# Optimization experiments

Measured on AMD Instinct MI355X. Metric: run time of the kernel, lower is better.

## Reference

```python
import jax, jax.numpy as jnp
import numpy as np

B, N, T = 1024, 8192, 11  # batch, max atoms, atom types


def setup_inputs() -> dict:
    key = jax.random.key(0)
    k1, k2, k3 = jax.random.split(key, 3)
    input_coords = jax.random.normal(k1, (B, 3 * N), dtype=jnp.float32)
    atom_types = jax.random.randint(k2, (B, N), 0, T, dtype=jnp.int32)
    num_atoms = jax.random.randint(k3, (B,), 0, N, dtype=jnp.int32)
    return {"input_coords": input_coords, "atom_types": atom_types, "num_atoms": num_atoms}


def reference(input_coords, atom_types, num_atoms):
    # input_coords: [B, 3N], atom_types: [B, N] in [0, T), num_atoms: [B]
    b, n3 = input_coords.shape
    n = n3 // 3
    valid = jnp.arange(n)[None, :] < num_atoms[:, None]          # [B, N]
    # padded atoms get a sentinel type T so they sort to the end
    t_eff = jnp.where(valid, atom_types, T)                       # [B, N]
    # stable sort by type = contiguous per-type buckets, original order kept within type
    perm = jnp.argsort(t_eff, axis=1)                             # [B, N] (stable)
    coords3 = input_coords.reshape(b, n, 3)
    out = jnp.take_along_axis(coords3, perm[:, :, None], axis=1)  # [B, N, 3]
    valid_sorted = jnp.take_along_axis(valid, perm, axis=1)       # [B, N]
    out = out * valid_sorted[:, :, None].astype(out.dtype)        # zero padded slots
    # per-type counts and exclusive-prefix offsets
    counts_all = jnp.sum(jax.nn.one_hot(t_eff, T + 1, dtype=jnp.int32), axis=1)  # [B, T+1]
    num_atoms_of_type = counts_all[:, :T]                         # [B, T]
    offsets = jnp.concatenate(
        [jnp.zeros((b, 1), jnp.int32), jnp.cumsum(num_atoms_of_type, axis=1)[:, :-1]], axis=1
    )                                                              # [B, T]
    return out.reshape(b, n3), num_atoms_of_type, offsets
```

## Files before the change

kernel.cpp:

```cpp
#include <hip/hip_runtime.h>

#define NB 512
#define APT 16
#define NTYPE 11
#define CPAD 13
#define NATOMS 8192
#define HALF 2048
#define NPASS (NATOMS / HALF)

__global__ __launch_bounds__(NB, 6)
void typed_coords_kernel(const float* __restrict__ coords,
                         const int*   __restrict__ types,
                         const int*   __restrict__ num_atoms,
                         float* __restrict__ out,
                         float* __restrict__ out_cnt,
                         float* __restrict__ out_off)
{
    const int b    = blockIdx.x;
    const int tid  = threadIdx.x;
    const int lane = tid & 63;
    const int wave = tid >> 6;

    __shared__ float lds_half[HALF * 3];
    __shared__ unsigned short lds_cnt[NB * CPAD];
    __shared__ int lds_counts[NTYPE];
    __shared__ int lds_off[NTYPE];

    const int na     = num_atoms[b];
    const int base_i = tid * APT;

    unsigned tp0 = 0, tp1 = 0;
    {
        const int* tptr = types + (size_t)b * NATOMS + base_i;
        if (base_i < na) {
            int4 a = reinterpret_cast<const int4*>(tptr)[0];
            int4 c = reinterpret_cast<const int4*>(tptr)[1];
            int4 e = reinterpret_cast<const int4*>(tptr)[2];
            int4 g = reinterpret_cast<const int4*>(tptr)[3];
            tp0 = (unsigned)a.x | ((unsigned)a.y << 4) | ((unsigned)a.z << 8)  | ((unsigned)a.w << 12)
                | ((unsigned)c.x << 16) | ((unsigned)c.y << 20) | ((unsigned)c.z << 24) | ((unsigned)c.w << 28);
            tp1 = (unsigned)e.x | ((unsigned)e.y << 4) | ((unsigned)e.z << 8)  | ((unsigned)e.w << 12)
                | ((unsigned)g.x << 16) | ((unsigned)g.y << 20) | ((unsigned)g.z << 24) | ((unsigned)g.w << 28);
        }
    }
#define TYP(k) ((int)((((k) < 8 ? tp0 : tp1) >> (((k) & 7) * 4)) & 0xFu))

    float cf[APT * 3];
    {
        const float4* c4 = reinterpret_cast<const float4*>(
            coords + (size_t)b * 3 * NATOMS + (size_t)base_i * 3);
        if (base_i < na) {
            #pragma unroll
            for (int g = 0; g < (APT * 3) / 4; ++g)
                *reinterpret_cast<float4*>(&cf[g * 4]) = c4[g];
        } else {
            #pragma unroll
            for (int i = 0; i < APT * 3; ++i) cf[i] = 0.0f;
        }
    }

    unsigned h0 = 0, h1 = 0, h2 = 0;
    if (base_i < na) {
        #pragma unroll
        for (int k = 0; k < APT; ++k) {
            if (base_i + k < na) {
                int t = TYP(k);
                int g = t >> 2;
                unsigned inc = 1u << ((t & 3) * 5);
                h0 += (g == 0) ? inc : 0u;
                h1 += (g == 1) ? inc : 0u;
                h2 += (g == 2) ? inc : 0u;
            }
        }
    }
    #pragma unroll
    for (int t = 0; t < NTYPE; ++t) {
        unsigned r = ((t >> 2) == 0) ? h0 : (((t >> 2) == 1) ? h1 : h2);
        lds_cnt[tid * CPAD + t] = (unsigned short)((r >> ((t & 3) * 5)) & 31u);
    }
    __syncthreads();

    for (int tt = wave; tt < NTYPE; tt += NB / 64) {
        int run = 0;
        #pragma unroll
        for (int s = 0; s < NB / 64; ++s) {
            int idx = (s * 64 + lane) * CPAD + tt;
            int v = lds_cnt[idx];
            int x = v;
            #pragma unroll
            for (int d = 1; d < 64; d <<= 1) {
                int n = __shfl_up(x, d);
                if (lane >= d) x += n;
            }
            lds_cnt[idx] = (unsigned short)(x - v + run);
            run += __shfl(x, 63);
        }
        lds_counts[tt] = run;
    }
    __syncthreads();

    if (tid == 0) {
        int acc = 0;
        #pragma unroll
        for (int t = 0; t < NTYPE; ++t) { lds_off[t] = acc; acc += lds_counts[t]; }
    }
    __syncthreads();

    if (tid < NTYPE) {
        out_cnt[(size_t)b * NTYPE + tid] = (float)lds_counts[tid];
        out_off[(size_t)b * NTYPE + tid] = (float)lds_off[tid];
    }

    unsigned dpk[APT / 2];
    #pragma unroll
    for (int h = 0; h < APT / 2; ++h) dpk[h] = 0xFFFFFFFFu;
    h0 = 0; h1 = 0; h2 = 0;
    if (base_i < na) {
        #pragma unroll
        for (int h = 0; h < APT / 2; ++h) {
            unsigned lo = 0xFFFFu, hi = 0xFFFFu;
            #pragma unroll
            for (int j = 0; j < 2; ++j) {
                int k = h * 2 + j;
                if (base_i + k < na) {
                    int t  = TYP(k);
                    int g  = t >> 2;
                    int sh = (t & 3) * 5;
                    unsigned cur  = (g == 0) ? h0 : ((g == 1) ? h1 : h2);
                    unsigned rank = (cur >> sh) & 31u;
                    unsigned base = lds_cnt[tid * CPAD + t];
                    unsigned d    = (unsigned)lds_off[t] + base + rank;
                    unsigned inc  = 1u << sh;
                    h0 += (g == 0) ? inc : 0u;
                    h1 += (g == 1) ? inc : 0u;
                    h2 += (g == 2) ? inc : 0u;
                    if (j == 0) lo = d; else hi = d;
                }
            }
            dpk[h] = lo | (hi << 16);
        }
    }

    #pragma unroll
    for (int i = 0; i < APT * 3; ++i) asm volatile("" : "+v"(cf[i]));

    #pragma unroll 1
    for (int p = 0; p < NPASS; ++p) {
        if (p) __syncthreads();

        float4* o4 = reinterpret_cast<float4*>(
            out + (size_t)b * 3 * NATOMS + (size_t)p * HALF * 3);

        if (na <= p * HALF) {
            float4 z = make_float4(0.f, 0.f, 0.f, 0.f);
            #pragma unroll
            for (int q = 0; q < (HALF * 3 / 4) / NB; ++q)
                o4[q * NB + tid] = z;
            continue;
        }

        int lo = na - p * HALF;
        if (lo < 0) lo = 0;
        if (lo > HALF) lo = HALF;
        for (int i = 3 * lo + tid; i < 3 * HALF; i += NB) lds_half[i] = 0.0f;

        #pragma unroll
        for (int h = 0; h < APT / 2; ++h) {
            unsigned pk = dpk[h];
            int d0 = (int)(pk & 0xFFFFu) - p * HALF;
            int d1 = (int)(pk >> 16)     - p * HALF;
            if (d0 >= 0 && d0 < HALF) {
                lds_half[d0 * 3 + 0] = cf[(h * 2 + 0) * 3 + 0];
                lds_half[d0 * 3 + 1] = cf[(h * 2 + 0) * 3 + 1];
                lds_half[d0 * 3 + 2] = cf[(h * 2 + 0) * 3 + 2];
            }
            if (d1 >= 0 && d1 < HALF) {
                lds_half[d1 * 3 + 0] = cf[(h * 2 + 1) * 3 + 0];
                lds_half[d1 * 3 + 1] = cf[(h * 2 + 1) * 3 + 1];
                lds_half[d1 * 3 + 2] = cf[(h * 2 + 1) * 3 + 2];
            }
        }
        __syncthreads();

        const float4* l4 = reinterpret_cast<const float4*>(lds_half);
        #pragma unroll
        for (int q = 0; q < (HALF * 3 / 4) / NB; ++q) {
            o4[q * NB + tid] = l4[q * NB + tid];
        }
    }
#undef TYP
}

extern "C" void kernel_launch(void* const* d_in, const int* in_sizes, int n_in,
                              void* d_out, int out_size, void* d_ws, size_t ws_size,
                              hipStream_t stream) {
    const float* coords = (const float*)d_in[0];
    const int*   types  = (const int*)d_in[1];
    const int*   nums   = (const int*)d_in[2];
    const int B = in_sizes[2];

    float* out     = (float*)d_out;
    float* out_cnt = out + (size_t)B * 3 * NATOMS;
    float* out_off = out_cnt + (size_t)B * NTYPE;

    typed_coords_kernel<<<B, NB, 0, stream>>>(coords, types, nums,
                                              out, out_cnt, out_off);
}
```

Baseline: 39.86 us.

## Replace LDS per-thread count scan with packed register wave scans and two-level offsets

Per-type counts are packed two per 32-bit register and scanned with wave shuffles across all types at once. A small second-level scan over the eight wave totals replaces the per-type LDS scan loop and the serial offset pass, removing one barrier and the large per-thread count array in shared memory. The freed LDS lets the staging buffer double to 4096 atoms, so the output is written in two passes instead of four, with fewer barriers. The cost is a larger staging buffer, which may reduce how many blocks fit per CU.

```diff
diff --git a/kernel.cpp b/kernel.cpp
--- a/kernel.cpp
+++ b/kernel.cpp
@@ -3,9 +3,8 @@
 #define NB 512
 #define APT 16
 #define NTYPE 11
-#define CPAD 13
 #define NATOMS 8192
-#define HALF 2048
+#define HALF 4096
 #define NPASS (NATOMS / HALF)
 
 __global__ __launch_bounds__(NB, 6)
@@ -21,10 +20,9 @@
     const int lane = tid & 63;
     const int wave = tid >> 6;
 
-    __shared__ float lds_half[HALF * 3];
-    __shared__ unsigned short lds_cnt[NB * CPAD];
-    __shared__ int lds_counts[NTYPE];
-    __shared__ int lds_off[NTYPE];
+    __shared__ float    lds_half[HALF * 3];
+    __shared__ unsigned lds_wtot[8][8];
+    __shared__ unsigned lds_pb[8][8];
 
     const int na     = num_atoms[b];
     const int base_i = tid * APT;
@@ -59,85 +57,111 @@
         }
     }
 
-    unsigned h0 = 0, h1 = 0, h2 = 0;
+    unsigned g0 = 0, g1 = 0, rpk0 = 0, rpk1 = 0;
     if (base_i < na) {
         #pragma unroll
         for (int k = 0; k < APT; ++k) {
             if (base_i + k < na) {
                 int t = TYP(k);
-                int g = t >> 2;
-                unsigned inc = 1u << ((t & 3) * 5);
-                h0 += (g == 0) ? inc : 0u;
-                h1 += (g == 1) ? inc : 0u;
-                h2 += (g == 2) ? inc : 0u;
-            }
-        }
-    }
+                bool c = t < 6;
+                int sh5 = (c ? t : t - 6) * 5;
+                unsigned cur  = c ? g0 : g1;
+                unsigned rank = (cur >> sh5) & 0xFu;
+                if (k < 8) rpk0 |= rank << (k * 4);
+                else       rpk1 |= rank << ((k - 8) * 4);
+                unsigned inc = 1u << sh5;
+                g0 += c ? inc : 0u;
+                g1 += c ? 0u : inc;
+            }
+        }
+    }
+
+    unsigned x[6], own[6];
+    #pragma unroll
+    for (int i = 0; i < 6; ++i) x[i] = 0;
     #pragma unroll
     for (int t = 0; t < NTYPE; ++t) {
-        unsigned r = ((t >> 2) == 0) ? h0 : (((t >> 2) == 1) ? h1 : h2);
-        lds_cnt[tid * CPAD + t] = (unsigned short)((r >> ((t & 3) * 5)) & 31u);
+        unsigned v = (((t < 6) ? g0 : g1) >> (((t < 6) ? t : t - 6) * 5)) & 31u;
+        x[t >> 1] |= v << ((t & 1) * 16);
+    }
+    #pragma unroll
+    for (int i = 0; i < 6; ++i) own[i] = x[i];
+
+    #pragma unroll
+    for (int d = 1; d < 64; d <<= 1) {
+        #pragma unroll
+        for (int i = 0; i < 6; ++i) {
+            unsigned n = __shfl_up(x[i], d);
+            if (lane >= d) x[i] += n;
+        }
+    }
+    unsigned e[6];
+    #pragma unroll
+    for (int i = 0; i < 6; ++i) e[i] = x[i] - own[i];
+    if (lane == 63) {
+        #pragma unroll
+        for (int i = 0; i < 6; ++i) lds_wtot[wave][i] = x[i];
     }
     __syncthreads();
 
-    for (int tt = wave; tt < NTYPE; tt += NB / 64) {
-        int run = 0;
-        #pragma unroll
-        for (int s = 0; s < NB / 64; ++s) {
-            int idx = (s * 64 + lane) * CPAD + tt;
-            int v = lds_cnt[idx];
-            int x = v;
-            #pragma unroll
-            for (int d = 1; d < 64; d <<= 1) {
-                int n = __shfl_up(x, d);
-                if (lane >= d) x += n;
-            }
-            lds_cnt[idx] = (unsigned short)(x - v + run);
-            run += __shfl(x, 63);
-        }
-        lds_counts[tt] = run;
+    if (wave == 0 && lane < 8) {
+        unsigned y[6], own2[6];
+        #pragma unroll
+        for (int i = 0; i < 6; ++i) { y[i] = lds_wtot[lane][i]; own2[i] = y[i]; }
+        #pragma unroll
+        for (int d = 1; d < 8; d <<= 1) {
+            #pragma unroll
+            for (int i = 0; i < 6; ++i) {
+                unsigned n = __shfl_up(y[i], d);
+                if (lane >= d) y[i] += n;
+            }
+        }
+        unsigned tot[6], ex2[6], offp[6];
+        #pragma unroll
+        for (int i = 0; i < 6; ++i) {
+            tot[i] = __shfl(y[i], 7);
+            ex2[i] = y[i] - own2[i];
+            offp[i] = 0;
+        }
+        unsigned acc = 0;
+        #pragma unroll
+        for (int t = 0; t < NTYPE; ++t) {
+            unsigned c = (tot[t >> 1] >> ((t & 1) * 16)) & 0xFFFFu;
+            offp[t >> 1] |= acc << ((t & 1) * 16);
+            if (lane == 0) {
+                out_cnt[(size_t)b * NTYPE + t] = (float)c;
+                out_off[(size_t)b * NTYPE + t] = (float)acc;
+            }
+            acc += c;
+        }
+        #pragma unroll
+        for (int i = 0; i < 6; ++i) lds_pb[lane][i] = offp[i] + ex2[i];
     }
     __syncthreads();
 
-    if (tid == 0) {
-        int acc = 0;
-        #pragma unroll
-        for (int t = 0; t < NTYPE; ++t) { lds_off[t] = acc; acc += lds_counts[t]; }
-    }
-    __syncthreads();
-
-    if (tid < NTYPE) {
-        out_cnt[(size_t)b * NTYPE + tid] = (float)lds_counts[tid];
-        out_off[(size_t)b * NTYPE + tid] = (float)lds_off[tid];
-    }
+    unsigned s[6];
+    #pragma unroll
+    for (int i = 0; i < 6; ++i) s[i] = lds_pb[wave][i] + e[i];
 
     unsigned dpk[APT / 2];
     #pragma unroll
     for (int h = 0; h < APT / 2; ++h) dpk[h] = 0xFFFFFFFFu;
-    h0 = 0; h1 = 0; h2 = 0;
     if (base_i < na) {
         #pragma unroll
-        for (int h = 0; h < APT / 2; ++h) {
-            unsigned lo = 0xFFFFu, hi = 0xFFFFu;
-            #pragma unroll
-            for (int j = 0; j < 2; ++j) {
-                int k = h * 2 + j;
-                if (base_i + k < na) {
-                    int t  = TYP(k);
-                    int g  = t >> 2;
-                    int sh = (t & 3) * 5;
-                    unsigned cur  = (g == 0) ? h0 : ((g == 1) ? h1 : h2);
-                    unsigned rank = (cur >> sh) & 31u;
-                    unsigned base = lds_cnt[tid * CPAD + t];
-                    unsigned d    = (unsigned)lds_off[t] + base + rank;
-                    unsigned inc  = 1u << sh;
-                    h0 += (g == 0) ? inc : 0u;
-                    h1 += (g == 1) ? inc : 0u;
-                    h2 += (g == 2) ? inc : 0u;
-                    if (j == 0) lo = d; else hi = d;
-                }
-            }
-            dpk[h] = lo | (hi << 16);
+        for (int k = 0; k < APT; ++k) {
+            if (base_i + k < na) {
+                int t = TYP(k);
+                int w = t >> 1;
+                unsigned u = (w < 2) ? ((w == 0) ? s[0] : s[1])
+                           : ((w < 4) ? ((w == 2) ? s[2] : s[3])
+                                      : ((w == 4) ? s[4] : s[5]));
+                unsigned base16 = (u >> ((t & 1) * 16)) & 0xFFFFu;
+                unsigned rank = ((k < 8) ? (rpk0 >> (k * 4))
+                                         : (rpk1 >> ((k - 8) * 4))) & 0xFu;
+                unsigned d = base16 + rank;
+                if (k & 1) dpk[k >> 1] = (dpk[k >> 1] & 0x0000FFFFu) | (d << 16);
+                else       dpk[k >> 1] = (dpk[k >> 1] & 0xFFFF0000u) | d;
+            }
         }
     }
 
```

After: 41.62 us. 1.04x slower.
